# Performance work log

Measured on AMD Instinct MI355X. Metric: run time of the kernel, lower is better.

Reference implementation:

```python
import jax, jax.numpy as jnp
import numpy as np
from math import sqrt

N_HEADS = 4
IN_FEATURES = 64
KQ = 64
HEAD_V = IN_FEATURES // N_HEADS  # 16


def setup_inputs() -> dict:
    key = jax.random.key(0)
    ks = jax.random.split(key, 7)
    s = 0.05
    x = jax.random.normal(ks[0], (8192, IN_FEATURES), dtype=jnp.float32)
    # Per-head Linear weights stacked on a leading head axis.
    # torch Linear: y = x @ W.T + b; we store W already transposed: [H, F, E]
    Wq = jax.random.normal(ks[1], (N_HEADS, IN_FEATURES, KQ), dtype=jnp.float32) * s
    bq = jax.random.normal(ks[2], (N_HEADS, KQ), dtype=jnp.float32) * s
    Wk = jax.random.normal(ks[3], (N_HEADS, IN_FEATURES, KQ), dtype=jnp.float32) * s
    bk = jax.random.normal(ks[4], (N_HEADS, KQ), dtype=jnp.float32) * s
    Wv = jax.random.normal(ks[5], (N_HEADS, IN_FEATURES, HEAD_V), dtype=jnp.float32) * s
    bv = jax.random.normal(ks[6], (N_HEADS, HEAD_V), dtype=jnp.float32) * s
    return {"x": x, "Wq": Wq, "bq": bq, "Wk": Wk, "bk": bk, "Wv": Wv, "bv": bv}


def reference(x, Wq, bq, Wk, bk, Wv, bv):
    N, F = x.shape
    scale = 1.0 / sqrt(F)  # original divides by sqrt(in_features), NOT sqrt(kq)
    # Batched-head projections: [H, N, E]
    Q = jnp.einsum('nf,hfe->hne', x, Wq) + bq[:, None, :]
    K = jnp.einsum('nf,hfe->hne', x, Wk) + bk[:, None, :]
    V = jnp.einsum('nf,hfd->hnd', x, Wv) + bv[:, None, :]
    logits = jnp.einsum('hne,hme->hnm', Q, K) * scale  # [H, N, N]
    attn = jax.nn.softmax(logits, axis=-1)
    out_heads = jnp.einsum('hnm,hmd->hnd', attn, V)    # [H, N, HEAD_V]
    # Head i writes columns [i*HEAD_V:(i+1)*HEAD_V] of the output.
    out = jnp.transpose(out_heads, (1, 0, 2)).reshape(N, F)
    return out
```

## Files before the change

kernel.cpp:

```cpp
#include <hip/hip_runtime.h>

typedef __attribute__((ext_vector_type(4))) float f32x4;
typedef __attribute__((ext_vector_type(8))) short bf16x8;
typedef __attribute__((ext_vector_type(4))) short bf16x4;
typedef long fp8x8;

#define NH 4

static __device__ __forceinline__ unsigned short f2bf(float f){
  unsigned u = __float_as_uint(f);
  u += 0x7FFFu + ((u >> 16) & 1u);
  return (unsigned short)(u >> 16);
}

static __device__ __forceinline__ unsigned pack2bf(float a, float b){
  return __builtin_amdgcn_perm(__float_as_uint(b) + 0x8000u,
                               __float_as_uint(a) + 0x8000u, 0x07060302u);
}

static __device__ __forceinline__ int pack_fp8x4(float a, float b, float c, float d){
  int w = __builtin_amdgcn_cvt_pk_fp8_f32(a, b, 0, false);
  w     = __builtin_amdgcn_cvt_pk_fp8_f32(c, d, w, true);
  return w;
}

__global__ __launch_bounds__(576) void proj_kernel(
    const float* __restrict__ x,
    const float* __restrict__ Wq, const float* __restrict__ bq,
    const float* __restrict__ Wk, const float* __restrict__ bk,
    const float* __restrict__ Wv, const float* __restrict__ bv,
    unsigned char* __restrict__ Qf8, unsigned char* __restrict__ Kt,
    unsigned short* __restrict__ Vt, int n)
{
  __shared__ float xsT[64*64];
  __shared__ float wqs[64*64];
  __shared__ float wks[64*64];
  __shared__ float wvs[64*16];
  __shared__ float bqs[64], bks[64], bvs[16];

  const int t  = threadIdx.x;
  const int h  = blockIdx.y;
  const int r0 = blockIdx.x * 64;

  const float4* xg = (const float4*)(x + (size_t)r0 * 64);
  for (int v = t; v < 1024; v += 576){
    float4 d4 = xg[v];
    int row = v >> 4, f0 = (v & 15) * 4;
    xsT[(f0+0)*64 + row] = d4.x;
    xsT[(f0+1)*64 + row] = d4.y;
    xsT[(f0+2)*64 + row] = d4.z;
    xsT[(f0+3)*64 + row] = d4.w;
  }
  const float4* wqg = (const float4*)(Wq + h*4096);
  const float4* wkg = (const float4*)(Wk + h*4096);
  for (int v = t; v < 1024; v += 576){
    ((float4*)wqs)[v] = wqg[v];
    ((float4*)wks)[v] = wkg[v];
  }
  if (t < 256) ((float4*)wvs)[t] = ((const float4*)(Wv + h*1024))[t];
  if (t < 64)       bqs[t]     = bq[h*64 + t];
  else if (t < 128) bks[t-64]  = bk[h*64 + (t-64)];
  else if (t < 144) bvs[t-128] = bv[h*16 + (t-128)];
  __syncthreads();

  const int r  = t & 63;
  const int cg = t >> 6;

  const float* wbase;
  int wstride;
  if (cg < 4)      { wbase = wqs + cg*16;     wstride = 64; }
  else if (cg < 8) { wbase = wks + (cg-4)*16; wstride = 64; }
  else             { wbase = wvs;             wstride = 16; }

  float acc[16];
  #pragma unroll
  for (int c = 0; c < 16; ++c) acc[c] = 0.f;

  for (int f = 0; f < 64; ++f){
    float xv = xsT[f*64 + r];
    const float4* w4 = (const float4*)(wbase + f*wstride);
    float4 w0 = w4[0], w1 = w4[1], w2 = w4[2], w3 = w4[3];
    acc[ 0] += xv*w0.x; acc[ 1] += xv*w0.y; acc[ 2] += xv*w0.z; acc[ 3] += xv*w0.w;
    acc[ 4] += xv*w1.x; acc[ 5] += xv*w1.y; acc[ 6] += xv*w1.z; acc[ 7] += xv*w1.w;
    acc[ 8] += xv*w2.x; acc[ 9] += xv*w2.y; acc[10] += xv*w2.z; acc[11] += xv*w2.w;
    acc[12] += xv*w3.x; acc[13] += xv*w3.y; acc[14] += xv*w3.z; acc[15] += xv*w3.w;
  }

  const float S1 = 0.4246609001f;
  const int gr  = r0 + r;
  const int tt  = gr >> 4;
  const int l16 = gr & 15;

  if (cg < 4){
    float v[16];
    #pragma unroll
    for (int c = 0; c < 16; ++c) v[c] = (acc[c] + bqs[cg*16 + c]) * S1;
    uint4 o;
    o.x = pack_fp8x4(v[ 0],v[ 1],v[ 2],v[ 3]);
    o.y = pack_fp8x4(v[ 4],v[ 5],v[ 6],v[ 7]);
    o.z = pack_fp8x4(v[ 8],v[ 9],v[10],v[11]);
    o.w = pack_fp8x4(v[12],v[13],v[14],v[15]);
    *(uint4*)(Qf8 + ((size_t)h*n + gr)*64 + cg*16) = o;
  } else if (cg < 8){
    const int c0 = (cg-4)*16;
    float v[16];
    #pragma unroll
    for (int c = 0; c < 16; ++c) v[c] = (acc[c] + bks[c0 + c]) * S1;
    uint4 o;
    o.x = pack_fp8x4(v[ 0],v[ 1],v[ 2],v[ 3]);
    o.y = pack_fp8x4(v[ 4],v[ 5],v[ 6],v[ 7]);
    o.z = pack_fp8x4(v[ 8],v[ 9],v[10],v[11]);
    o.w = pack_fp8x4(v[12],v[13],v[14],v[15]);
    const int hf = (cg-4) >> 1;
    const int qp = ((cg-4) & 1) * 2;
    unsigned char* base = Kt + (size_t)h*((size_t)n<<6) + (size_t)tt*1024 + hf*8;
    *(uint2*)(base + ((qp  )*16 + l16)*16) = make_uint2(o.x, o.y);
    *(uint2*)(base + ((qp+1)*16 + l16)*16) = make_uint2(o.z, o.w);
  } else {
    const int qd = (gr >> 2) & 3;
    const int j  = gr & 3;
    unsigned short* base = Vt + (size_t)h*((size_t)n<<4) + (size_t)tt*256 + j;
    #pragma unroll
    for (int c = 0; c < 16; ++c)
      base[(qd*16 + c)*4] = f2bf(acc[c] + bvs[c]);
  }
}

__global__ __launch_bounds__(1024, 4) void attn_kernel(
    const unsigned char* __restrict__ Qf8, const unsigned char* __restrict__ Kt,
    const unsigned short* __restrict__ Vt, float* __restrict__ out, int n)
{
  __shared__ float part[12][64][17];

  const int tid  = threadIdx.x;
  const int lane = tid & 63;
  const int w    = tid >> 6;
  const int wr   = w & 3;
  const int jq   = w >> 2;
  const int bid  = blockIdx.x;
  const int h    = bid & 3;
  const int iblk = bid >> 2;
  const int l16  = lane & 15, quad = lane >> 4;
  const int i0   = iblk*128 + wr*32;
  const int ntiles = (n >> 2) >> 4;
  const int tile0  = jq * ntiles;

  const unsigned char* qbase = Qf8 + ((size_t)h*n + i0 + l16)*64 + quad*8;
  fp8x8 qf00 = *(const fp8x8*)(qbase);
  fp8x8 qf01 = *(const fp8x8*)(qbase + 32);
  fp8x8 qf10 = *(const fp8x8*)(qbase + 16*64);
  fp8x8 qf11 = *(const fp8x8*)(qbase + 16*64 + 32);

  const uint4* ktu = (const uint4*)(Kt + (size_t)h*((size_t)n<<6)) + (size_t)tile0*64 + lane;
  const uint2* vtu = (const uint2*)(Vt + (size_t)h*((size_t)n<<4)) + (size_t)tile0*64 + lane;

  f32x4 o0  = {0.f,0.f,0.f,0.f};
  f32x4 o1  = {0.f,0.f,0.f,0.f};
  f32x4 la0 = {0.f,0.f,0.f,0.f};
  f32x4 la1 = {0.f,0.f,0.f,0.f};
  const f32x4 z = {0.f,0.f,0.f,0.f};
  const bf16x4 vones = {(short)0x3F80, (short)0x3F80, (short)0x3F80, (short)0x3F80};

  uint4 ka = ktu[0];
  uint2 va = vtu[0];
  uint4 kb = ktu[64];
  uint2 vb = vtu[64];

  for (int tt = 0; tt < ntiles; tt += 2){
    int tn = tt + 2; if (tn >= ntiles) tn = 0;
    uint4 kc = ktu[(size_t)tn*64];
    uint2 vc = vtu[(size_t)tn*64];
    uint4 kd = ktu[(size_t)(tn+1)*64];
    uint2 vd = vtu[(size_t)(tn+1)*64];

    {
      fp8x8 k0 = (fp8x8)(((unsigned long long)ka.y << 32) | ka.x);
      fp8x8 k1 = (fp8x8)(((unsigned long long)ka.w << 32) | ka.z);
      bf16x4 vf; { union { uint2 u; bf16x4 v; } c; c.u = va; vf = c.v; }

      f32x4 s0 = __builtin_amdgcn_mfma_f32_16x16x32_fp8_fp8(k0, qf00, z, 0, 0, 0);
      s0 = __builtin_amdgcn_mfma_f32_16x16x32_fp8_fp8(k1, qf01, s0, 0, 0, 0);
      f32x4 s1 = __builtin_amdgcn_mfma_f32_16x16x32_fp8_fp8(k0, qf10, z, 0, 0, 0);
      s1 = __builtin_amdgcn_mfma_f32_16x16x32_fp8_fp8(k1, qf11, s1, 0, 0, 0);

      float p00 = __builtin_amdgcn_exp2f(s0[0]);
      float p01 = __builtin_amdgcn_exp2f(s0[1]);
      float p02 = __builtin_amdgcn_exp2f(s0[2]);
      float p03 = __builtin_amdgcn_exp2f(s0[3]);
      float p10 = __builtin_amdgcn_exp2f(s1[0]);
      float p11 = __builtin_amdgcn_exp2f(s1[1]);
      float p12 = __builtin_amdgcn_exp2f(s1[2]);
      float p13 = __builtin_amdgcn_exp2f(s1[3]);

      union { uint2 u; bf16x4 v; } pc0, pc1;
      pc0.u = make_uint2(pack2bf(p00,p01), pack2bf(p02,p03));
      pc1.u = make_uint2(pack2bf(p10,p11), pack2bf(p12,p13));
      o0  = __builtin_amdgcn_mfma_f32_16x16x16bf16_1k(pc0.v, vf,    o0,  0, 0, 0);
      o1  = __builtin_amdgcn_mfma_f32_16x16x16bf16_1k(pc1.v, vf,    o1,  0, 0, 0);
      la0 = __builtin_amdgcn_mfma_f32_16x16x16bf16_1k(pc0.v, vones, la0, 0, 0, 0);
      la1 = __builtin_amdgcn_mfma_f32_16x16x16bf16_1k(pc1.v, vones, la1, 0, 0, 0);
    }
    {
      fp8x8 k0 = (fp8x8)(((unsigned long long)kb.y << 32) | kb.x);
      fp8x8 k1 = (fp8x8)(((unsigned long long)kb.w << 32) | kb.z);
      bf16x4 vf; { union { uint2 u; bf16x4 v; } c; c.u = vb; vf = c.v; }

      f32x4 s0 = __builtin_amdgcn_mfma_f32_16x16x32_fp8_fp8(k0, qf00, z, 0, 0, 0);
      s0 = __builtin_amdgcn_mfma_f32_16x16x32_fp8_fp8(k1, qf01, s0, 0, 0, 0);
      f32x4 s1 = __builtin_amdgcn_mfma_f32_16x16x32_fp8_fp8(k0, qf10, z, 0, 0, 0);
      s1 = __builtin_amdgcn_mfma_f32_16x16x32_fp8_fp8(k1, qf11, s1, 0, 0, 0);

      float p00 = __builtin_amdgcn_exp2f(s0[0]);
      float p01 = __builtin_amdgcn_exp2f(s0[1]);
      float p02 = __builtin_amdgcn_exp2f(s0[2]);
      float p03 = __builtin_amdgcn_exp2f(s0[3]);
      float p10 = __builtin_amdgcn_exp2f(s1[0]);
      float p11 = __builtin_amdgcn_exp2f(s1[1]);
      float p12 = __builtin_amdgcn_exp2f(s1[2]);
      float p13 = __builtin_amdgcn_exp2f(s1[3]);

      union { uint2 u; bf16x4 v; } pc0, pc1;
      pc0.u = make_uint2(pack2bf(p00,p01), pack2bf(p02,p03));
      pc1.u = make_uint2(pack2bf(p10,p11), pack2bf(p12,p13));
      o0  = __builtin_amdgcn_mfma_f32_16x16x16bf16_1k(pc0.v, vf,    o0,  0, 0, 0);
      o1  = __builtin_amdgcn_mfma_f32_16x16x16bf16_1k(pc1.v, vf,    o1,  0, 0, 0);
      la0 = __builtin_amdgcn_mfma_f32_16x16x16bf16_1k(pc0.v, vones, la0, 0, 0, 0);
      la1 = __builtin_amdgcn_mfma_f32_16x16x16bf16_1k(pc1.v, vones, la1, 0, 0, 0);
    }

    ka = kc; va = vc;
    kb = kd; vb = vd;
  }

  if (w >= 4){
    float* p = &part[w-4][lane][0];
    p[ 0]=o0[0];  p[ 1]=o0[1];  p[ 2]=o0[2];  p[ 3]=o0[3];
    p[ 4]=o1[0];  p[ 5]=o1[1];  p[ 6]=o1[2];  p[ 7]=o1[3];
    p[ 8]=la0[0]; p[ 9]=la0[1]; p[10]=la0[2]; p[11]=la0[3];
    p[12]=la1[0]; p[13]=la1[1]; p[14]=la1[2]; p[15]=la1[3];
  }
  __syncthreads();

  if (w < 4){
    #pragma unroll
    for (int q = 0; q < 3; ++q){
      const float* r = &part[w + 4*q][lane][0];
      o0[0] +=r[0];  o0[1] +=r[1];  o0[2] +=r[2];  o0[3] +=r[3];
      o1[0] +=r[4];  o1[1] +=r[5];  o1[2] +=r[6];  o1[3] +=r[7];
      la0[0]+=r[8];  la0[1]+=r[9];  la0[2]+=r[10]; la0[3]+=r[11];
      la1[0]+=r[12]; la1[1]+=r[13]; la1[2]+=r[14]; la1[3]+=r[15];
    }
    #pragma unroll
    for (int reg = 0; reg < 4; ++reg){
      int i = quad*4 + reg;
      out[(size_t)(i0 + i)*64      + h*16 + l16] = o0[reg] / la0[reg];
      out[(size_t)(i0 + 16 + i)*64 + h*16 + l16] = o1[reg] / la1[reg];
    }
  }
}

extern "C" void kernel_launch(void* const* d_in, const int* in_sizes, int n_in,
                              void* d_out, int out_size, void* d_ws, size_t ws_size,
                              hipStream_t stream) {
  const float* x  = (const float*)d_in[0];
  const float* Wq = (const float*)d_in[1];
  const float* bq = (const float*)d_in[2];
  const float* Wk = (const float*)d_in[3];
  const float* bk = (const float*)d_in[4];
  const float* Wv = (const float*)d_in[5];
  const float* bv = (const float*)d_in[6];
  float* out = (float*)d_out;

  const int n = in_sizes[0] / 64;

  unsigned char* Qf8 = (unsigned char*)d_ws;
  unsigned char* Kt  = Qf8 + (size_t)NH * n * 64;
  unsigned short* Vt = (unsigned short*)(Kt + (size_t)NH * n * 64);

  proj_kernel<<<dim3(n/64, NH), 576, 0, stream>>>(x, Wq, bq, Wk, bk, Wv, bv, Qf8, Kt, Vt, n);
  attn_kernel<<<dim3((n/128)*NH), 1024, 0, stream>>>(Qf8, Kt, Vt, out, n);
}
```

Measured before the change: 135.7 us.

## Use bf16 MFMA for projections with prepacked weights; shrink attention blocks

Adds a weight-prep kernel that folds the softmax scale into the weights, converts them to bf16 and packs them into MFMA operand layout. The projection kernel then runs on bf16 MFMA instructions instead of scalar FP32 FMAs, and writes Q in a transposed layout. The attention kernel drops from 1024 threads per block covering 128 rows to 512 threads covering 64 rows, which doubles the grid, and it gathers Q bytes with strided loads. The aim is cheaper projection math and better occupancy in attention, at the cost of an extra launch, lower projection precision and less efficient Q loads.

Result: no change. 133.3 us (-1.8%).

```diff
diff --git a/kernel.cpp b/kernel.cpp
--- a/kernel.cpp
+++ b/kernel.cpp
@@ -24,132 +24,200 @@
   return w;
 }
 
-__global__ __launch_bounds__(576) void proj_kernel(
-    const float* __restrict__ x,
+__global__ __launch_bounds__(256) void wprep_kernel(
     const float* __restrict__ Wq, const float* __restrict__ bq,
     const float* __restrict__ Wk, const float* __restrict__ bk,
-    const float* __restrict__ Wv, const float* __restrict__ bv,
-    unsigned char* __restrict__ Qf8, unsigned char* __restrict__ Kt,
+    const float* __restrict__ Wv,
+    unsigned short* __restrict__ WF, float* __restrict__ bias_s, int n)
+{
+  __shared__ unsigned short wqT[64*72];
+  __shared__ unsigned short wkT[64*72];
+  __shared__ unsigned short wvT[16*72];
+
+  const int t = threadIdx.x;
+  const int h = blockIdx.x;
+  const float S1 = 0.4246609001f;
+  const int f = t >> 2, eg = t & 3;
+
+  {
+    const float4* g = (const float4*)(Wq + h*4096 + f*64 + eg*16);
+    #pragma unroll
+    for (int p = 0; p < 4; ++p){
+      float4 d = g[p];
+      int e0 = eg*16 + p*4;
+      wqT[(e0+0)*72 + f] = f2bf(d.x * S1);
+      wqT[(e0+1)*72 + f] = f2bf(d.y * S1);
+      wqT[(e0+2)*72 + f] = f2bf(d.z * S1);
+      wqT[(e0+3)*72 + f] = f2bf(d.w * S1);
+    }
+  }
+  {
+    const float4* g = (const float4*)(Wk + h*4096 + f*64 + eg*16);
+    #pragma unroll
+    for (int p = 0; p < 4; ++p){
+      float4 d = g[p];
+      int e0 = eg*16 + p*4;
+      wkT[(e0+0)*72 + f] = f2bf(d.x * S1);
+      wkT[(e0+1)*72 + f] = f2bf(d.y * S1);
+      wkT[(e0+2)*72 + f] = f2bf(d.z * S1);
+      wkT[(e0+3)*72 + f] = f2bf(d.w * S1);
+    }
+  }
+  {
+    float4 d = *(const float4*)(Wv + h*1024 + f*16 + eg*4);
+    int d0 = eg*4;
+    wvT[(d0+0)*72 + f] = f2bf(d.x);
+    wvT[(d0+1)*72 + f] = f2bf(d.y);
+    wvT[(d0+2)*72 + f] = f2bf(d.z);
+    wvT[(d0+3)*72 + f] = f2bf(d.w);
+  }
+  if (t < 64)       bias_s[h*128 + t] = bq[h*64 + t] * S1;
+  else if (t < 128) bias_s[h*128 + t] = bk[h*64 + (t-64)] * S1;
+  __syncthreads();
+
+  const int lane = t & 63, w = t >> 6;
+  const int quad = lane >> 4, l16 = lane & 15;
+  for (int s = w; s < 18; s += 4){
+    const unsigned short* src;
+    if (s < 8){      int jt = s>>1,     ks = s&1;     src = wqT + (jt*16+l16)*72 + ks*32 + quad*8; }
+    else if (s < 16){int ft = (s-8)>>1, ks = (s-8)&1; src = wkT + (ft*16+l16)*72 + ks*32 + quad*8; }
+    else {           int ks = s-16;                   src = wvT + l16*72 + ks*32 + quad*8; }
+    uint4 v = *(const uint4*)src;
+    *(uint4*)(WF + ((size_t)(h*18 + s)*64 + lane)*8) = v;
+  }
+}
+
+__global__ __launch_bounds__(256) void proj_kernel(
+    const float* __restrict__ x, const float* __restrict__ bv,
+    const unsigned short* __restrict__ WF, const float* __restrict__ bias_s,
+    unsigned char* __restrict__ Qt, unsigned char* __restrict__ Kt,
     unsigned short* __restrict__ Vt, int n)
 {
-  __shared__ float xsT[64*64];
-  __shared__ float wqs[64*64];
-  __shared__ float wks[64*64];
-  __shared__ float wvs[64*16];
-  __shared__ float bqs[64], bks[64], bvs[16];
+  __shared__ unsigned short xf[8*64*8];
+  __shared__ float bql[64], bkl[64], bvl[16];
 
   const int t  = threadIdx.x;
   const int h  = blockIdx.y;
   const int r0 = blockIdx.x * 64;
 
-  const float4* xg = (const float4*)(x + (size_t)r0 * 64);
-  for (int v = t; v < 1024; v += 576){
-    float4 d4 = xg[v];
-    int row = v >> 4, f0 = (v & 15) * 4;
-    xsT[(f0+0)*64 + row] = d4.x;
-    xsT[(f0+1)*64 + row] = d4.y;
-    xsT[(f0+2)*64 + row] = d4.z;
-    xsT[(f0+3)*64 + row] = d4.w;
-  }
-  const float4* wqg = (const float4*)(Wq + h*4096);
-  const float4* wkg = (const float4*)(Wk + h*4096);
-  for (int v = t; v < 1024; v += 576){
-    ((float4*)wqs)[v] = wqg[v];
-    ((float4*)wks)[v] = wkg[v];
-  }
-  if (t < 256) ((float4*)wvs)[t] = ((const float4*)(Wv + h*1024))[t];
-  if (t < 64)       bqs[t]     = bq[h*64 + t];
-  else if (t < 128) bks[t-64]  = bk[h*64 + (t-64)];
-  else if (t < 144) bvs[t-128] = bv[h*16 + (t-128)];
+  {
+    const int r = t >> 2, cg4 = t & 3;
+    const float4* g = (const float4*)(x + (size_t)(r0 + r)*64 + cg4*16);
+    float4 a = g[0], b = g[1], c = g[2], d = g[3];
+    unsigned u0 = pack2bf(a.x,a.y), u1 = pack2bf(a.z,a.w);
+    unsigned u2 = pack2bf(b.x,b.y), u3 = pack2bf(b.z,b.w);
+    unsigned u4 = pack2bf(c.x,c.y), u5 = pack2bf(c.z,c.w);
+    unsigned u6 = pack2bf(d.x,d.y), u7 = pack2bf(d.z,d.w);
+    const int it = r >> 4, l16r = r & 15, ks = cg4 >> 1, q0 = (cg4 & 1)*2;
+    uint4* dst0 = (uint4*)(xf + ((it*2+ks)*64 + q0*16     + l16r)*8);
+    uint4* dst1 = (uint4*)(xf + ((it*2+ks)*64 + (q0+1)*16 + l16r)*8);
+    *dst0 = make_uint4(u0,u1,u2,u3);
+    *dst1 = make_uint4(u4,u5,u6,u7);
+  }
+  if (t < 64)        bql[t]     = bias_s[h*128 + t];
+  else if (t < 128)  bkl[t-64]  = bias_s[h*128 + t];
+  else if (t < 144)  bvl[t-128] = bv[h*16 + (t-128)];
   __syncthreads();
 
-  const int r  = t & 63;
-  const int cg = t >> 6;
-
-  const float* wbase;
-  int wstride;
-  if (cg < 4)      { wbase = wqs + cg*16;     wstride = 64; }
-  else if (cg < 8) { wbase = wks + (cg-4)*16; wstride = 64; }
-  else             { wbase = wvs;             wstride = 16; }
-
-  float acc[16];
-  #pragma unroll
-  for (int c = 0; c < 16; ++c) acc[c] = 0.f;
-
-  for (int f = 0; f < 64; ++f){
-    float xv = xsT[f*64 + r];
-    const float4* w4 = (const float4*)(wbase + f*wstride);
-    float4 w0 = w4[0], w1 = w4[1], w2 = w4[2], w3 = w4[3];
-    acc[ 0] += xv*w0.x; acc[ 1] += xv*w0.y; acc[ 2] += xv*w0.z; acc[ 3] += xv*w0.w;
-    acc[ 4] += xv*w1.x; acc[ 5] += xv*w1.y; acc[ 6] += xv*w1.z; acc[ 7] += xv*w1.w;
-    acc[ 8] += xv*w2.x; acc[ 9] += xv*w2.y; acc[10] += xv*w2.z; acc[11] += xv*w2.w;
-    acc[12] += xv*w3.x; acc[13] += xv*w3.y; acc[14] += xv*w3.z; acc[15] += xv*w3.w;
-  }
-
-  const float S1 = 0.4246609001f;
-  const int gr  = r0 + r;
-  const int tt  = gr >> 4;
-  const int l16 = gr & 15;
-
-  if (cg < 4){
-    float v[16];
-    #pragma unroll
-    for (int c = 0; c < 16; ++c) v[c] = (acc[c] + bqs[cg*16 + c]) * S1;
-    uint4 o;
-    o.x = pack_fp8x4(v[ 0],v[ 1],v[ 2],v[ 3]);
-    o.y = pack_fp8x4(v[ 4],v[ 5],v[ 6],v[ 7]);
-    o.z = pack_fp8x4(v[ 8],v[ 9],v[10],v[11]);
-    o.w = pack_fp8x4(v[12],v[13],v[14],v[15]);
-    *(uint4*)(Qf8 + ((size_t)h*n + gr)*64 + cg*16) = o;
-  } else if (cg < 8){
-    const int c0 = (cg-4)*16;
-    float v[16];
-    #pragma unroll
-    for (int c = 0; c < 16; ++c) v[c] = (acc[c] + bks[c0 + c]) * S1;
-    uint4 o;
-    o.x = pack_fp8x4(v[ 0],v[ 1],v[ 2],v[ 3]);
-    o.y = pack_fp8x4(v[ 4],v[ 5],v[ 6],v[ 7]);
-    o.z = pack_fp8x4(v[ 8],v[ 9],v[10],v[11]);
-    o.w = pack_fp8x4(v[12],v[13],v[14],v[15]);
-    const int hf = (cg-4) >> 1;
-    const int qp = ((cg-4) & 1) * 2;
-    unsigned char* base = Kt + (size_t)h*((size_t)n<<6) + (size_t)tt*1024 + hf*8;
-    *(uint2*)(base + ((qp  )*16 + l16)*16) = make_uint2(o.x, o.y);
-    *(uint2*)(base + ((qp+1)*16 + l16)*16) = make_uint2(o.z, o.w);
-  } else {
-    const int qd = (gr >> 2) & 3;
-    const int j  = gr & 3;
-    unsigned short* base = Vt + (size_t)h*((size_t)n<<4) + (size_t)tt*256 + j;
-    #pragma unroll
-    for (int c = 0; c < 16; ++c)
-      base[(qd*16 + c)*4] = f2bf(acc[c] + bvs[c]);
-  }
-}
-
-__global__ __launch_bounds__(1024, 4) void attn_kernel(
-    const unsigned char* __restrict__ Qf8, const unsigned char* __restrict__ Kt,
+  const int lane = t & 63, w = t >> 6;
+  const int quad = lane >> 4, l16 = lane & 15;
+
+  bf16x8 xa[8];
+  #pragma unroll
+  for (int i = 0; i < 8; ++i)
+    xa[i] = *(const bf16x8*)(xf + (i*64 + lane)*8);
+
+  const unsigned short* WFh = WF + (size_t)h*18*64*8;
+  bf16x8 wq[8];
+  #pragma unroll
+  for (int s = 0; s < 8; ++s)
+    wq[s] = *(const bf16x8*)(WFh + ((size_t)s*64 + lane)*8);
+  bf16x8 wk0 = *(const bf16x8*)(WFh + ((size_t)(8 + w*2 + 0)*64 + lane)*8);
+  bf16x8 wk1 = *(const bf16x8*)(WFh + ((size_t)(8 + w*2 + 1)*64 + lane)*8);
+  bf16x8 wv0 = *(const bf16x8*)(WFh + ((size_t)16*64 + lane)*8);
+  bf16x8 wv1 = *(const bf16x8*)(WFh + ((size_t)17*64 + lane)*8);
+
+  const f32x4 z = {0.f,0.f,0.f,0.f};
+  f32x4 accQ[4] = {z,z,z,z};
+  f32x4 accK[4] = {z,z,z,z};
+  f32x4 accV = z;
+
+  #pragma unroll
+  for (int jt = 0; jt < 4; ++jt){
+    accQ[jt] = __builtin_amdgcn_mfma_f32_16x16x32_bf16(xa[w*2+0], wq[jt*2+0], accQ[jt], 0,0,0);
+    accQ[jt] = __builtin_amdgcn_mfma_f32_16x16x32_bf16(xa[w*2+1], wq[jt*2+1], accQ[jt], 0,0,0);
+  }
+  #pragma unroll
+  for (int tt = 0; tt < 4; ++tt){
+    accK[tt] = __builtin_amdgcn_mfma_f32_16x16x32_bf16(wk0, xa[tt*2+0], accK[tt], 0,0,0);
+    accK[tt] = __builtin_amdgcn_mfma_f32_16x16x32_bf16(wk1, xa[tt*2+1], accK[tt], 0,0,0);
+  }
+  accV = __builtin_amdgcn_mfma_f32_16x16x32_bf16(xa[w*2+0], wv0, accV, 0,0,0);
+  accV = __builtin_amdgcn_mfma_f32_16x16x32_bf16(xa[w*2+1], wv1, accV, 0,0,0);
+
+  #pragma unroll
+  for (int jt = 0; jt < 4; ++jt){
+    float bqv = bql[jt*16 + l16];
+    unsigned o = pack_fp8x4(accQ[jt][0]+bqv, accQ[jt][1]+bqv,
+                            accQ[jt][2]+bqv, accQ[jt][3]+bqv);
+    *(unsigned*)(Qt + ((size_t)(h*64 + jt*16 + l16))*n + r0 + w*16 + quad*4) = o;
+  }
+  {
+    const int f0 = w*16 + quad*4;
+    const float bk0 = bkl[f0], bk1 = bkl[f0+1], bk2 = bkl[f0+2], bk3 = bkl[f0+3];
+    const int qk = (f0 & 31) >> 3, hf = f0 >> 5, boff = (quad & 1) * 4;
+    #pragma unroll
+    for (int tt = 0; tt < 4; ++tt){
+      unsigned o = pack_fp8x4(accK[tt][0]+bk0, accK[tt][1]+bk1,
+                              accK[tt][2]+bk2, accK[tt][3]+bk3);
+      const int T = (r0 >> 4) + tt;
+      *(unsigned*)(Kt + (size_t)h*((size_t)n<<6) + (size_t)T*1024
+                      + (qk*16 + l16)*16 + hf*8 + boff) = o;
+    }
+  }
+  {
+    float bvv = bvl[l16];
+    unsigned v01 = pack2bf(accV[0]+bvv, accV[1]+bvv);
+    unsigned v23 = pack2bf(accV[2]+bvv, accV[3]+bvv);
+    const int T = (r0 >> 4) + w;
+    *(uint2*)(Vt + (size_t)h*((size_t)n<<4) + ((size_t)T*64 + lane)*4) = make_uint2(v01, v23);
+  }
+}
+
+__global__ __launch_bounds__(512) void attn_kernel(
+    const unsigned char* __restrict__ Qt, const unsigned char* __restrict__ Kt,
     const unsigned short* __restrict__ Vt, float* __restrict__ out, int n)
 {
-  __shared__ float part[12][64][17];
+  __shared__ float part[6][64][17];
 
   const int tid  = threadIdx.x;
   const int lane = tid & 63;
   const int w    = tid >> 6;
-  const int wr   = w & 3;
-  const int jq   = w >> 2;
+  const int rg   = w >> 2;
+  const int jq   = w & 3;
   const int bid  = blockIdx.x;
   const int h    = bid & 3;
   const int iblk = bid >> 2;
   const int l16  = lane & 15, quad = lane >> 4;
-  const int i0   = iblk*128 + wr*32;
+  const int i0   = iblk*64 + rg*32;
   const int ntiles = (n >> 2) >> 4;
   const int tile0  = jq * ntiles;
 
-  const unsigned char* qbase = Qf8 + ((size_t)h*n + i0 + l16)*64 + quad*8;
-  fp8x8 qf00 = *(const fp8x8*)(qbase);
-  fp8x8 qf01 = *(const fp8x8*)(qbase + 32);
-  fp8x8 qf10 = *(const fp8x8*)(qbase + 16*64);
-  fp8x8 qf11 = *(const fp8x8*)(qbase + 16*64 + 32);
+  const unsigned char* qh = Qt + (size_t)(h*64)*n;
+  fp8x8 qf[4];
+  #pragma unroll
+  for (int v = 0; v < 4; ++v){
+    const int row0 = i0 + (v >> 1)*16;
+    const int kb   = (v & 1)*32;
+    const unsigned char* qp = qh + (size_t)(kb + quad*8)*n + row0 + l16;
+    unsigned u0 = 0, u1 = 0;
+    #pragma unroll
+    for (int j = 0; j < 4; ++j) u0 |= (unsigned)qp[(size_t)j*n] << (8*j);
+    #pragma unroll
+    for (int j = 0; j < 4; ++j) u1 |= (unsigned)qp[(size_t)(j+4)*n] << (8*j);
+    qf[v] = (fp8x8)(((unsigned long long)u1 << 32) | (unsigned long long)u0);
+  }
+  const fp8x8 qf00 = qf[0], qf01 = qf[1], qf10 = qf[2], qf11 = qf[3];
 
   const uint4* ktu = (const uint4*)(Kt + (size_t)h*((size_t)n<<6)) + (size_t)tile0*64 + lane;
   const uint2* vtu = (const uint2*)(Vt + (size_t)h*((size_t)n<<4)) + (size_t)tile0*64 + lane;
@@ -232,8 +300,8 @@
     kb = kd; vb = vd;
   }
 
-  if (w >= 4){
-    float* p = &part[w-4][lane][0];
+  if (jq > 0){
+    float* p = &part[rg*3 + (jq-1)][lane][0];
     p[ 0]=o0[0];  p[ 1]=o0[1];  p[ 2]=o0[2];  p[ 3]=o0[3];
     p[ 4]=o1[0];  p[ 5]=o1[1];  p[ 6]=o1[2];  p[ 7]=o1[3];
     p[ 8]=la0[0]; p[ 9]=la0[1]; p[10]=la0[2]; p[11]=la0[3];
@@ -241,10 +309,10 @@
   }
   __syncthreads();
 
-  if (w < 4){
+  if (jq == 0){
     #pragma unroll
     for (int q = 0; q < 3; ++q){
-      const float* r = &part[w + 4*q][lane][0];
+      const float* r = &part[rg*3 + q][lane][0];
       o0[0] +=r[0];  o0[1] +=r[1];  o0[2] +=r[2];  o0[3] +=r[3];
       o1[0] +=r[4];  o1[1] +=r[5];  o1[2] +=r[6];  o1[3] +=r[7];
       la0[0]+=r[8];  la0[1]+=r[9];  la0[2]+=r[10]; la0[3]+=r[11];
@@ -273,10 +341,13 @@
 
   const int n = in_sizes[0] / 64;
 
-  unsigned char* Qf8 = (unsigned char*)d_ws;
-  unsigned char* Kt  = Qf8 + (size_t)NH * n * 64;
-  unsigned short* Vt = (unsigned short*)(Kt + (size_t)NH * n * 64);
-
-  proj_kernel<<<dim3(n/64, NH), 576, 0, stream>>>(x, Wq, bq, Wk, bk, Wv, bv, Qf8, Kt, Vt, n);
-  attn_kernel<<<dim3((n/128)*NH), 1024, 0, stream>>>(Qf8, Kt, Vt, out, n);
-}
+  unsigned char* Qt   = (unsigned char*)d_ws;
+  unsigned char* Kt   = Qt + (size_t)NH*64*n;
+  unsigned short* Vt  = (unsigned short*)(Kt + (size_t)NH*n*64);
+  unsigned short* WF  = Vt + (size_t)NH*n*16;
+  float* bias_s       = (float*)(WF + (size_t)NH*18*64*8);
+
+  wprep_kernel<<<NH, 256, 0, stream>>>(Wq, bq, Wk, bk, Wv, WF, bias_s, n);
+  proj_kernel<<<dim3(n/64, NH), 256, 0, stream>>>(x, bv, WF, bias_s, Qt, Kt, Vt, n);
+  attn_kernel<<<dim3((n/64)*NH), 512, 0, stream>>>(Qt, Kt, Vt, out, n);
+}
```
